# Optimization experiments

Hardware: AMD Instinct MI355X
Metric: run time of the kernel (lower is better)

Reference implementation:

```python
import jax, jax.numpy as jnp
import numpy as np

N = 100000
E = 3200000
NEG_SLOPE = 0.2  # PyG GATConv default


def gat_layer(x, src, dst, W, a_src, a_dst, b, heads, out_ch, concat):
    # per-node linear transform, split into heads: [N, H, C]
    h = (x @ W).reshape(N, heads, out_ch)
    # per-node attention logits: [N, H]
    al_src = jnp.sum(h * a_src, axis=-1)
    al_dst = jnp.sum(h * a_dst, axis=-1)
    # per-edge attention coefficient (x_j = source, x_i = target): [E, H]
    e = jax.nn.leaky_relu(al_src[src] + al_dst[dst], NEG_SLOPE)
    # segment softmax over incoming edges of each destination node
    m = jax.ops.segment_max(e, dst, num_segments=N)
    e = jnp.exp(e - m[dst])
    denom = jax.ops.segment_sum(e, dst, num_segments=N)
    alpha = e / (denom[dst] + 1e-16)
    # weighted message aggregation: scatter-add over dst
    msg = h[src] * alpha[..., None]  # [E, H, C]
    out = jax.ops.segment_sum(msg, dst, num_segments=N)  # [N, H, C]
    out = out.reshape(N, heads * out_ch) if concat else out.mean(axis=1)
    return out + b


def setup_inputs() -> dict:
    key = jax.random.key(0)
    ks = jax.random.split(key, 11)
    return {
        "x": jax.random.normal(ks[0], (N, 2), dtype=jnp.float32),
        "edge_index": jax.random.randint(ks[1], (2, E), 0, N, dtype=jnp.int64),
        "edge_attr": jax.random.normal(ks[2], (E, 1), dtype=jnp.float32),
        "W1": jax.random.normal(ks[3], (2, 32), dtype=jnp.float32) * 0.5,
        "att_src1": jax.random.normal(ks[4], (4, 8), dtype=jnp.float32) * 0.3,
        "att_dst1": jax.random.normal(ks[5], (4, 8), dtype=jnp.float32) * 0.3,
        "b1": jnp.zeros((32,), dtype=jnp.float32),
        "W2": jax.random.normal(ks[6], (32, 2), dtype=jnp.float32) * 0.2,
        "att_src2": jax.random.normal(ks[7], (1, 2), dtype=jnp.float32) * 0.3,
        "att_dst2": jax.random.normal(ks[8], (1, 2), dtype=jnp.float32) * 0.3,
        "b2": jnp.zeros((2,), dtype=jnp.float32),
    }


def reference(x, edge_index, edge_attr, W1, att_src1, att_dst1, b1, W2, att_src2, att_dst2, b2):
    # add self-loops (PyG GATConv default add_self_loops=True)
    loops = jnp.arange(N, dtype=edge_index.dtype)
    src = jnp.concatenate([edge_index[0], loops])
    dst = jnp.concatenate([edge_index[1], loops])
    h = gat_layer(x, src, dst, W1, att_src1, att_dst1, b1, heads=4, out_ch=8, concat=True)
    h = jax.nn.elu(h)
    out = gat_layer(h, src, dst, W2, att_src2, att_dst2, b2, heads=1, out_ch=2, concat=False)
    return out
```

## Files before the change

kernel.cpp:

```cpp
#include <hip/hip_runtime.h>
#include <math.h>

#define NEG_SLOPE 0.2f
#define BK_BITS 8
#define BK (1 << BK_BITS)
#define SBITS 17
#define SMASK ((1 << SBITS) - 1)
#define CAP 9216
#define PPT1 9
#define SW(p) ((p) ^ (((p) >> 5) & 31))
#define BCUR(b) ((b) * 16)

__device__ __forceinline__ float lrelu(float x) { return x > 0.f ? x : NEG_SLOPE * x; }

__global__ __launch_bounds__(512) void bucket_scatter(const int* __restrict__ src,
                                                      const int* __restrict__ dst,
                                                      int* __restrict__ bcur,
                                                      int* __restrict__ pairs, int E) {
    __shared__ int cnt[512], off[512], cur[512], adj[512];
    __shared__ int2 lpair[8196];
    __shared__ int sTot;
    int t = threadIdx.x;
    cnt[t] = 0;
    __syncthreads();

    int E4 = E >> 2;
    const int4* src4 = (const int4*)src;
    const int4* dst4 = (const int4*)dst;
    int base4 = blockIdx.x * 2048;
    int4 d4[4], s4[4];
    bool val[4];
#pragma unroll
    for (int k = 0; k < 4; k++) {
        int i4 = base4 + k * 512 + t;
        val[k] = (i4 < E4);
        if (val[k]) { d4[k] = dst4[i4]; s4[k] = src4[i4]; }
    }
    int dt = -1, st = 0;
    if (blockIdx.x == gridDim.x - 1) {
        int e = (E4 << 2) + t;
        if (e < E) { dt = dst[e]; st = src[e]; }
    }
#pragma unroll
    for (int k = 0; k < 4; k++) {
        if (val[k]) {
            atomicAdd(&cnt[d4[k].x >> BK_BITS], 1);
            atomicAdd(&cnt[d4[k].y >> BK_BITS], 1);
            atomicAdd(&cnt[d4[k].z >> BK_BITS], 1);
            atomicAdd(&cnt[d4[k].w >> BK_BITS], 1);
        }
    }
    if (dt >= 0) atomicAdd(&cnt[dt >> BK_BITS], 1);
    __syncthreads();

    if (t < 64) {
        int v[8], mysum = 0;
#pragma unroll
        for (int k = 0; k < 8; k++) { v[k] = cnt[t * 8 + k]; mysum += v[k]; }
        int s = mysum;
#pragma unroll
        for (int o = 1; o < 64; o <<= 1) {
            int u = __shfl_up(s, o);
            if (t >= o) s += u;
        }
        int run = s - mysum;
#pragma unroll
        for (int k = 0; k < 8; k++) {
            int d2 = t * 8 + k;
            off[d2] = run; cur[d2] = run;
            run += v[k];
        }
        if (t == 63) sTot = s;
    }
    __syncthreads();
    if (cnt[t] > 0) {
        int g0 = atomicAdd(&bcur[BCUR(t)], cnt[t]);
        adj[t] = t * CAP + g0 - off[t];
    }
    __syncthreads();
    int total = sTot;

#pragma unroll
    for (int k = 0; k < 4; k++) {
        if (val[k]) {
            int slot;
            slot = atomicAdd(&cur[d4[k].x >> BK_BITS], 1); lpair[slot] = make_int2(d4[k].x, s4[k].x);
            slot = atomicAdd(&cur[d4[k].y >> BK_BITS], 1); lpair[slot] = make_int2(d4[k].y, s4[k].y);
            slot = atomicAdd(&cur[d4[k].z >> BK_BITS], 1); lpair[slot] = make_int2(d4[k].z, s4[k].z);
            slot = atomicAdd(&cur[d4[k].w >> BK_BITS], 1); lpair[slot] = make_int2(d4[k].w, s4[k].w);
        }
    }
    if (dt >= 0) {
        int slot = atomicAdd(&cur[dt >> BK_BITS], 1);
        lpair[slot] = make_int2(dt, st);
    }
    __syncthreads();

    for (int i = t; i < total; i += 512) {
        int2 e = lpair[i];
        int b = e.x >> BK_BITS;
        pairs[adj[b] + i] = ((e.x & (BK - 1)) << SBITS) | e.y;
    }
}

__global__ __launch_bounds__(1024) void agg1_sortgather(
        const int* __restrict__ pairs, const int* __restrict__ bcur,
        const float2* __restrict__ x2,
        const float* __restrict__ W1, const float* __restrict__ asrc,
        const float* __restrict__ adst, const float* __restrict__ b1,
        const float* __restrict__ W2, const float* __restrict__ as2,
        const float* __restrict__ ad2,
        float2* __restrict__ h2, float* __restrict__ al2d,
        int* __restrict__ rowdeg, int* __restrict__ pairs_out, int N) {
    __shared__ float sW[64], sB[32], sW2[64], sP[4], sQ[4], sPd[4], sQd[4], sA2[4];
    __shared__ int cnt[BK], off[BK], cur[BK];
    __shared__ int sorted[CAP];
    int t = threadIdx.x;
    int b = blockIdx.x;
    if (t < 64) { sW[t] = W1[t]; sW2[t] = W2[t]; }
    if (t < 32) sB[t] = b1[t];
    if (t < 2) { sA2[t] = as2[t]; sA2[2 + t] = ad2[t]; }
    if (t >= 64 && t < 68) {
        int tt = t - 64;
        float P = 0.f, Q = 0.f, Pd = 0.f, Qd = 0.f;
#pragma unroll
        for (int k = 0; k < 8; k++) {
            int c = tt * 8 + k;
            float a = asrc[c], ad_ = adst[c];
            float w0 = W1[c], w1 = W1[32 + c];
            P += w0 * a; Q += w1 * a;
            Pd += w0 * ad_; Qd += w1 * ad_;
        }
        sP[tt] = P; sQ[tt] = Q; sPd[tt] = Pd; sQd[tt] = Qd;
    }
    if (t < BK) cnt[t] = 0;
    __syncthreads();

    int dbase = b << BK_BITS;
    int ndst = min(BK, N - dbase);
    int lo = b * CAP;
    int hi = lo + min(bcur[BCUR(b)], CAP);

    int myp[PPT1];
#pragma unroll
    for (int k = 0; k < PPT1; k++) {
        int i = lo + t + k * 1024;
        myp[k] = (i < hi) ? pairs[i] : -1;
    }
#pragma unroll
    for (int k = 0; k < PPT1; k++) {
        if (myp[k] >= 0) atomicAdd(&cnt[myp[k] >> SBITS], 1);
    }
    __syncthreads();

    if (t < 64) {
        int v[4], mysum = 0;
#pragma unroll
        for (int k = 0; k < 4; k++) { v[k] = cnt[t * 4 + k]; mysum += v[k]; }
        int s = mysum;
#pragma unroll
        for (int o = 1; o < 64; o <<= 1) {
            int u = __shfl_up(s, o);
            if (t >= o) s += u;
        }
        int run = s - mysum;
#pragma unroll
        for (int k = 0; k < 4; k++) {
            int d2 = t * 4 + k;
            off[d2] = run; cur[d2] = run;
            run += v[k];
        }
    }
    __syncthreads();

#pragma unroll
    for (int k = 0; k < PPT1; k++) {
        int p = myp[k];
        if (p >= 0) {
            int pos = atomicAdd(&cur[p >> SBITS], 1);
            sorted[SW(pos)] = p & SMASK;
        }
    }
    __syncthreads();

    {
        const int4* s4 = (const int4*)sorted;
        int4* p4 = (int4*)(pairs_out + lo);
        for (int i = t; i < CAP / 4; i += 1024) p4[i] = s4[i];
    }
    if (t < ndst) rowdeg[dbase + t] = (off[t] << 8) | min(cnt[t], 255);

    int d = t >> 2, q = t & 3;
    if (d < ndst) {
        int n = dbase + d;
        float rP[4], rQ[4], ald[4];
        float2 xd = x2[n];
#pragma unroll
        for (int h = 0; h < 4; h++) {
            rP[h] = sP[h]; rQ[h] = sQ[h];
            ald[h] = xd.x * sPd[h] + xd.y * sQd[h];
        }
        int deg = cnt[d];
        int start = off[d];
        int ids[16];
#pragma unroll
        for (int k = 0; k < 16; k++) {
            int j = q + 4 * k;
            ids[k] = (j < deg) ? sorted[SW(start + j)] : -1;
        }
        float Sw[4] = {0.f, 0.f, 0.f, 0.f};
        float S0[4] = {0.f, 0.f, 0.f, 0.f};
        float S1[4] = {0.f, 0.f, 0.f, 0.f};
#pragma unroll
        for (int half = 0; half < 2; half++) {
            float2 xv[8];
#pragma unroll
            for (int k = 0; k < 8; k++) {
                int id = ids[half * 8 + k];
                xv[k] = x2[id >= 0 ? id : 0];
            }
#pragma unroll
            for (int k = 0; k < 8; k++) {
                if (ids[half * 8 + k] >= 0) {
#pragma unroll
                    for (int h = 0; h < 4; h++) {
                        float e = lrelu(fmaf(xv[k].x, rP[h], fmaf(xv[k].y, rQ[h], ald[h])));
                        float w = __expf(fminf(e, 80.f));
                        Sw[h] += w; S0[h] += w * xv[k].x; S1[h] += w * xv[k].y;
                    }
                }
            }
        }
        for (int j = q + 64; j < deg; j += 4) {
            int s = sorted[SW(start + j)];
            float2 xs = x2[s];
#pragma unroll
            for (int h = 0; h < 4; h++) {
                float e = lrelu(fmaf(xs.x, rP[h], fmaf(xs.y, rQ[h], ald[h])));
                float w = __expf(fminf(e, 80.f));
                Sw[h] += w; S0[h] += w * xs.x; S1[h] += w * xs.y;
            }
        }
#pragma unroll
        for (int o = 1; o <= 2; o <<= 1) {
#pragma unroll
            for (int h = 0; h < 4; h++) {
                Sw[h] += __shfl_xor(Sw[h], o);
                S0[h] += __shfl_xor(S0[h], o);
                S1[h] += __shfl_xor(S1[h], o);
            }
        }
        if (q == 0) {
#pragma unroll
            for (int h = 0; h < 4; h++) {
                float e = lrelu(fmaf(xd.x, rP[h], fmaf(xd.y, rQ[h], ald[h])));
                float w = __expf(fminf(e, 80.f));
                Sw[h] += w; S0[h] += w * xd.x; S1[h] += w * xd.y;
            }
            float r[4];
#pragma unroll
            for (int h = 0; h < 4; h++) r[h] = 1.f / (Sw[h] + 1e-16f);
            float h20 = 0.f, h21 = 0.f;
#pragma unroll
            for (int c = 0; c < 32; c++) {
                int h = c >> 3;
                float outc = (sW[c] * S0[h] + sW[32 + c] * S1[h]) * r[h];
                float v2 = outc + sB[c];
                v2 = v2 > 0.f ? v2 : __expf(v2) - 1.f;
                h20 = fmaf(v2, sW2[2 * c], h20);
                h21 = fmaf(v2, sW2[2 * c + 1], h21);
            }
            h2[n] = make_float2(h20, h21);
            al2d[n] = h20 * sA2[2] + h21 * sA2[3];
        }
    }
}

__global__ __launch_bounds__(1024) void agg2_gather(
        const int* __restrict__ pairs, const int* __restrict__ rowdeg,
        const float2* __restrict__ h2, const float* __restrict__ al2d,
        const float* __restrict__ as2, const float* __restrict__ b2,
        float2* __restrict__ out, int N) {
    __shared__ int sorted[CAP];
    int t = threadIdx.x;
    int b = blockIdx.x;
    int dbase = b << BK_BITS;
    int ndst = min(BK, N - dbase);
    int lo = b * CAP;
    float a0 = as2[0], a1 = as2[1];

    {
        const int4* p4 = (const int4*)(pairs + lo);
        int4* s4 = (int4*)sorted;
        for (int i = t; i < CAP / 4; i += 1024) s4[i] = p4[i];
    }
    __syncthreads();

    int d = t >> 2, q = t & 3;
    if (d < ndst) {
        int n = dbase + d;
        int rd = rowdeg[n];
        int start = rd >> 8;
        int deg = rd & 255;
        float ald = al2d[n];
        float2 hd = h2[n];
        int ids[16];
#pragma unroll
        for (int k = 0; k < 16; k++) {
            int j = q + 4 * k;
            ids[k] = (j < deg) ? sorted[SW(start + j)] : -1;
        }
        float wsum = 0.f, ax = 0.f, ay = 0.f;
#pragma unroll
        for (int half = 0; half < 2; half++) {
            float2 hv[8];
#pragma unroll
            for (int k = 0; k < 8; k++) {
                int id = ids[half * 8 + k];
                hv[k] = h2[id >= 0 ? id : 0];
            }
#pragma unroll
            for (int k = 0; k < 8; k++) {
                if (ids[half * 8 + k] >= 0) {
                    float e = lrelu(fmaf(hv[k].x, a0, fmaf(hv[k].y, a1, ald)));
                    float w = __expf(fminf(e, 80.f));
                    wsum += w; ax = fmaf(w, hv[k].x, ax); ay = fmaf(w, hv[k].y, ay);
                }
            }
        }
        for (int j = q + 64; j < deg; j += 4) {
            int s = sorted[SW(start + j)];
            float2 hv = h2[s];
            float e = lrelu(fmaf(hv.x, a0, fmaf(hv.y, a1, ald)));
            float w = __expf(fminf(e, 80.f));
            wsum += w; ax = fmaf(w, hv.x, ax); ay = fmaf(w, hv.y, ay);
        }
#pragma unroll
        for (int o = 1; o <= 2; o <<= 1) {
            wsum += __shfl_xor(wsum, o);
            ax += __shfl_xor(ax, o);
            ay += __shfl_xor(ay, o);
        }
        if (q == 0) {
            float e = lrelu(fmaf(hd.x, a0, fmaf(hd.y, a1, ald)));
            float w = __expf(fminf(e, 80.f));
            wsum += w; ax = fmaf(w, hd.x, ax); ay = fmaf(w, hd.y, ay);
            float inv = 1.f / (wsum + 1e-16f);
            out[n] = make_float2(ax * inv + b2[0], ay * inv + b2[1]);
        }
    }
}

extern "C" void kernel_launch(void* const* d_in, const int* in_sizes, int n_in,
                              void* d_out, int out_size, void* d_ws, size_t ws_size,
                              hipStream_t stream) {
    const float* x     = (const float*)d_in[0];
    const int*   eidx  = (const int*)d_in[1];
    const float* W1    = (const float*)d_in[3];
    const float* asrc1 = (const float*)d_in[4];
    const float* adst1 = (const float*)d_in[5];
    const float* b1    = (const float*)d_in[6];
    const float* W2    = (const float*)d_in[7];
    const float* asrc2 = (const float*)d_in[8];
    const float* adst2 = (const float*)d_in[9];
    const float* b2    = (const float*)d_in[10];

    const int N = in_sizes[0] / 2;
    const int E = in_sizes[1] / 2;
    const int* src = eidx;
    const int* dst = eidx + E;
    const int NB = (N + BK - 1) >> BK_BITS;

    float* w = (float*)d_ws;
    float2* h2    = (float2*)w;
    float*  al2d  = w + 2 * (size_t)N;
    int* ip       = (int*)(w + 3 * (size_t)N);
    int* rowdeg   = ip;
    int* bcur     = ip + (size_t)N;
    int* pairs    = ip + (size_t)N + 8192;

    int E4 = E >> 2;
    int gS = (E4 + 2047) / 2048;

    hipMemsetAsync(bcur, 0, 8192 * sizeof(int), stream);
    bucket_scatter<<<gS, 512, 0, stream>>>(src, dst, bcur, pairs, E);
    agg1_sortgather<<<NB, 1024, 0, stream>>>(pairs, bcur, (const float2*)x,
                                             W1, asrc1, adst1, b1, W2, asrc2, adst2,
                                             h2, al2d, rowdeg, pairs, N);
    agg2_gather<<<NB, 1024, 0, stream>>>(pairs, rowdeg, (const float2*)h2, al2d,
                                         asrc2, b2, (float2*)d_out, N);
}
```

Baseline: 161.6 us.

## Replace global bucket atomics with per-block fixed cells and drop memset

The scatter kernel no longer reserves space in each destination bucket with global atomics. Each scatter block writes its edges into a fixed 64-slot cell per bucket and records its per-bucket count, and the aggregation kernel reads all cells for its bucket using those counts. This removes the memset launch and the contention on global atomics, but it reads up to nblk*64 slots per bucket (26 rounds per thread) and silently drops any edges beyond 64 per cell. The second-layer kernel now reads the sorted lists straight from global memory instead of staging them in LDS, removing a block-wide barrier.

```diff
diff --git a/kernel.cpp b/kernel.cpp
--- a/kernel.cpp
+++ b/kernel.cpp
@@ -7,27 +7,29 @@
 #define SBITS 17
 #define SMASK ((1 << SBITS) - 1)
 #define CAP 9216
-#define PPT1 9
+#define CELL 64
+#define RNDS 26
 #define SW(p) ((p) ^ (((p) >> 5) & 31))
-#define BCUR(b) ((b) * 16)
 
 __device__ __forceinline__ float lrelu(float x) { return x > 0.f ? x : NEG_SLOPE * x; }
 
 __global__ __launch_bounds__(512) void bucket_scatter(const int* __restrict__ src,
                                                       const int* __restrict__ dst,
-                                                      int* __restrict__ bcur,
-                                                      int* __restrict__ pairs, int E) {
-    __shared__ int cnt[512], off[512], cur[512], adj[512];
+                                                      int* __restrict__ cnt_g,
+                                                      int* __restrict__ cells,
+                                                      int E, int nblk) {
+    __shared__ int cnt[512], off[512], cur[512];
     __shared__ int2 lpair[8196];
     __shared__ int sTot;
     int t = threadIdx.x;
+    int blk = blockIdx.x;
     cnt[t] = 0;
     __syncthreads();
 
     int E4 = E >> 2;
     const int4* src4 = (const int4*)src;
     const int4* dst4 = (const int4*)dst;
-    int base4 = blockIdx.x * 2048;
+    int base4 = blk * 2048;
     int4 d4[4], s4[4];
     bool val[4];
 #pragma unroll
@@ -37,7 +39,7 @@
         if (val[k]) { d4[k] = dst4[i4]; s4[k] = src4[i4]; }
     }
     int dt = -1, st = 0;
-    if (blockIdx.x == gridDim.x - 1) {
+    if (blk == gridDim.x - 1) {
         int e = (E4 << 2) + t;
         if (e < E) { dt = dst[e]; st = src[e]; }
     }
@@ -53,6 +55,7 @@
     if (dt >= 0) atomicAdd(&cnt[dt >> BK_BITS], 1);
     __syncthreads();
 
+    cnt_g[blk * 512 + t] = min(cnt[t], CELL);
     if (t < 64) {
         int v[8], mysum = 0;
 #pragma unroll
@@ -71,11 +74,6 @@
             run += v[k];
         }
         if (t == 63) sTot = s;
-    }
-    __syncthreads();
-    if (cnt[t] > 0) {
-        int g0 = atomicAdd(&bcur[BCUR(t)], cnt[t]);
-        adj[t] = t * CAP + g0 - off[t];
     }
     __syncthreads();
     int total = sTot;
@@ -96,24 +94,29 @@
     }
     __syncthreads();
 
+    int cellbase = blk * CELL;
     for (int i = t; i < total; i += 512) {
         int2 e = lpair[i];
         int b = e.x >> BK_BITS;
-        pairs[adj[b] + i] = ((e.x & (BK - 1)) << SBITS) | e.y;
+        int slot = i - off[b];
+        if (slot < CELL)
+            cells[(size_t)b * (nblk * CELL) + cellbase + slot] =
+                ((e.x & (BK - 1)) << SBITS) | e.y;
     }
 }
 
 __global__ __launch_bounds__(1024) void agg1_sortgather(
-        const int* __restrict__ pairs, const int* __restrict__ bcur,
+        const int* __restrict__ cells, const int* __restrict__ cnt_g,
         const float2* __restrict__ x2,
         const float* __restrict__ W1, const float* __restrict__ asrc,
         const float* __restrict__ adst, const float* __restrict__ b1,
         const float* __restrict__ W2, const float* __restrict__ as2,
         const float* __restrict__ ad2,
         float2* __restrict__ h2, float* __restrict__ al2d,
-        int* __restrict__ rowdeg, int* __restrict__ pairs_out, int N) {
+        int* __restrict__ rowdeg, int* __restrict__ pairs2, int N, int nblk) {
     __shared__ float sW[64], sB[32], sW2[64], sP[4], sQ[4], sPd[4], sQd[4], sA2[4];
     __shared__ int cnt[BK], off[BK], cur[BK];
+    __shared__ int ccnt[512];
     __shared__ int sorted[CAP];
     int t = threadIdx.x;
     int b = blockIdx.x;
@@ -133,23 +136,25 @@
         }
         sP[tt] = P; sQ[tt] = Q; sPd[tt] = Pd; sQd[tt] = Qd;
     }
-    if (t < BK) cnt[t] = 0;
+    if (t < nblk) ccnt[t] = cnt_g[t * 512 + b];
+    if (t >= 512 && t < 512 + BK) cnt[t - 512] = 0;
     __syncthreads();
 
     int dbase = b << BK_BITS;
     int ndst = min(BK, N - dbase);
-    int lo = b * CAP;
-    int hi = lo + min(bcur[BCUR(b)], CAP);
-
-    int myp[PPT1];
-#pragma unroll
-    for (int k = 0; k < PPT1; k++) {
-        int i = lo + t + k * 1024;
-        myp[k] = (i < hi) ? pairs[i] : -1;
-    }
-#pragma unroll
-    for (int k = 0; k < PPT1; k++) {
-        if (myp[k] >= 0) atomicAdd(&cnt[myp[k] >> SBITS], 1);
+    int nslots = nblk * CELL;
+    size_t base = (size_t)b * nslots;
+
+    int myp[RNDS];
+#pragma unroll
+    for (int r = 0; r < RNDS; r++) {
+        int s = t + r * 1024;
+        bool v = (s < nslots) && ((s & (CELL - 1)) < ccnt[s >> 6]);
+        myp[r] = v ? cells[base + s] : -1;
+    }
+#pragma unroll
+    for (int r = 0; r < RNDS; r++) {
+        if (myp[r] >= 0) atomicAdd(&cnt[myp[r] >> SBITS], 1);
     }
     __syncthreads();
 
@@ -174,8 +179,8 @@
     __syncthreads();
 
 #pragma unroll
-    for (int k = 0; k < PPT1; k++) {
-        int p = myp[k];
+    for (int r = 0; r < RNDS; r++) {
+        int p = myp[r];
         if (p >= 0) {
             int pos = atomicAdd(&cur[p >> SBITS], 1);
             sorted[SW(pos)] = p & SMASK;
@@ -183,11 +188,7 @@
     }
     __syncthreads();
 
-    {
-        const int4* s4 = (const int4*)sorted;
-        int4* p4 = (int4*)(pairs_out + lo);
-        for (int i = t; i < CAP / 4; i += 1024) p4[i] = s4[i];
-    }
+    for (int i = t; i < CAP; i += 1024) pairs2[b * CAP + i] = sorted[SW(i)];
     if (t < ndst) rowdeg[dbase + t] = (off[t] << 8) | min(cnt[t], 255);
 
     int d = t >> 2, q = t & 3;
@@ -277,77 +278,68 @@
 }
 
 __global__ __launch_bounds__(1024) void agg2_gather(
-        const int* __restrict__ pairs, const int* __restrict__ rowdeg,
+        const int* __restrict__ pairs2, const int* __restrict__ rowdeg,
         const float2* __restrict__ h2, const float* __restrict__ al2d,
         const float* __restrict__ as2, const float* __restrict__ b2,
         float2* __restrict__ out, int N) {
-    __shared__ int sorted[CAP];
     int t = threadIdx.x;
     int b = blockIdx.x;
     int dbase = b << BK_BITS;
     int ndst = min(BK, N - dbase);
-    int lo = b * CAP;
+    int d = t >> 2, q = t & 3;
+    if (d >= ndst) return;
     float a0 = as2[0], a1 = as2[1];
 
-    {
-        const int4* p4 = (const int4*)(pairs + lo);
-        int4* s4 = (int4*)sorted;
-        for (int i = t; i < CAP / 4; i += 1024) s4[i] = p4[i];
-    }
-    __syncthreads();
-
-    int d = t >> 2, q = t & 3;
-    if (d < ndst) {
-        int n = dbase + d;
-        int rd = rowdeg[n];
-        int start = rd >> 8;
-        int deg = rd & 255;
-        float ald = al2d[n];
-        float2 hd = h2[n];
-        int ids[16];
-#pragma unroll
-        for (int k = 0; k < 16; k++) {
-            int j = q + 4 * k;
-            ids[k] = (j < deg) ? sorted[SW(start + j)] : -1;
-        }
-        float wsum = 0.f, ax = 0.f, ay = 0.f;
-#pragma unroll
-        for (int half = 0; half < 2; half++) {
-            float2 hv[8];
-#pragma unroll
-            for (int k = 0; k < 8; k++) {
-                int id = ids[half * 8 + k];
-                hv[k] = h2[id >= 0 ? id : 0];
-            }
-#pragma unroll
-            for (int k = 0; k < 8; k++) {
-                if (ids[half * 8 + k] >= 0) {
-                    float e = lrelu(fmaf(hv[k].x, a0, fmaf(hv[k].y, a1, ald)));
-                    float w = __expf(fminf(e, 80.f));
-                    wsum += w; ax = fmaf(w, hv[k].x, ax); ay = fmaf(w, hv[k].y, ay);
-                }
-            }
-        }
-        for (int j = q + 64; j < deg; j += 4) {
-            int s = sorted[SW(start + j)];
-            float2 hv = h2[s];
-            float e = lrelu(fmaf(hv.x, a0, fmaf(hv.y, a1, ald)));
-            float w = __expf(fminf(e, 80.f));
-            wsum += w; ax = fmaf(w, hv.x, ax); ay = fmaf(w, hv.y, ay);
-        }
-#pragma unroll
-        for (int o = 1; o <= 2; o <<= 1) {
-            wsum += __shfl_xor(wsum, o);
-            ax += __shfl_xor(ax, o);
-            ay += __shfl_xor(ay, o);
-        }
-        if (q == 0) {
-            float e = lrelu(fmaf(hd.x, a0, fmaf(hd.y, a1, ald)));
-            float w = __expf(fminf(e, 80.f));
-            wsum += w; ax = fmaf(w, hd.x, ax); ay = fmaf(w, hd.y, ay);
-            float inv = 1.f / (wsum + 1e-16f);
-            out[n] = make_float2(ax * inv + b2[0], ay * inv + b2[1]);
-        }
+    int n = dbase + d;
+    int rd = rowdeg[n];
+    int start = rd >> 8;
+    int deg = rd & 255;
+    const int* lst = pairs2 + b * CAP + start;
+    float ald = al2d[n];
+    float2 hd = h2[n];
+    int ids[16];
+#pragma unroll
+    for (int k = 0; k < 16; k++) {
+        int j = q + 4 * k;
+        ids[k] = (j < deg) ? lst[j] : -1;
+    }
+    float wsum = 0.f, ax = 0.f, ay = 0.f;
+#pragma unroll
+    for (int half = 0; half < 2; half++) {
+        float2 hv[8];
+#pragma unroll
+        for (int k = 0; k < 8; k++) {
+            int id = ids[half * 8 + k];
+            hv[k] = h2[id >= 0 ? id : 0];
+        }
+#pragma unroll
+        for (int k = 0; k < 8; k++) {
+            if (ids[half * 8 + k] >= 0) {
+                float e = lrelu(fmaf(hv[k].x, a0, fmaf(hv[k].y, a1, ald)));
+                float w = __expf(fminf(e, 80.f));
+                wsum += w; ax = fmaf(w, hv[k].x, ax); ay = fmaf(w, hv[k].y, ay);
+            }
+        }
+    }
+    for (int j = q + 64; j < deg; j += 4) {
+        int s = lst[j];
+        float2 hv = h2[s];
+        float e = lrelu(fmaf(hv.x, a0, fmaf(hv.y, a1, ald)));
+        float w = __expf(fminf(e, 80.f));
+        wsum += w; ax = fmaf(w, hv.x, ax); ay = fmaf(w, hv.y, ay);
+    }
+#pragma unroll
+    for (int o = 1; o <= 2; o <<= 1) {
+        wsum += __shfl_xor(wsum, o);
+        ax += __shfl_xor(ax, o);
+        ay += __shfl_xor(ay, o);
+    }
+    if (q == 0) {
+        float e = lrelu(fmaf(hd.x, a0, fmaf(hd.y, a1, ald)));
+        float w = __expf(fminf(e, 80.f));
+        wsum += w; ax = fmaf(w, hd.x, ax); ay = fmaf(w, hd.y, ay);
+        float inv = 1.f / (wsum + 1e-16f);
+        out[n] = make_float2(ax * inv + b2[0], ay * inv + b2[1]);
     }
 }
 
@@ -370,23 +362,22 @@
     const int* src = eidx;
     const int* dst = eidx + E;
     const int NB = (N + BK - 1) >> BK_BITS;
+    int E4 = E >> 2;
+    const int nblk = (E4 + 2047) / 2048;
 
     float* w = (float*)d_ws;
     float2* h2    = (float2*)w;
     float*  al2d  = w + 2 * (size_t)N;
     int* ip       = (int*)(w + 3 * (size_t)N);
     int* rowdeg   = ip;
-    int* bcur     = ip + (size_t)N;
-    int* pairs    = ip + (size_t)N + 8192;
-
-    int E4 = E >> 2;
-    int gS = (E4 + 2047) / 2048;
-
-    hipMemsetAsync(bcur, 0, 8192 * sizeof(int), stream);
-    bucket_scatter<<<gS, 512, 0, stream>>>(src, dst, bcur, pairs, E);
-    agg1_sortgather<<<NB, 1024, 0, stream>>>(pairs, bcur, (const float2*)x,
+    int* cnt_g    = ip + (size_t)N;
+    int* pairs2   = cnt_g + (size_t)nblk * 512;
+    int* cells    = pairs2 + (size_t)NB * CAP;
+
+    bucket_scatter<<<nblk, 512, 0, stream>>>(src, dst, cnt_g, cells, E, nblk);
+    agg1_sortgather<<<NB, 1024, 0, stream>>>(cells, cnt_g, (const float2*)x,
                                              W1, asrc1, adst1, b1, W2, asrc2, adst2,
-                                             h2, al2d, rowdeg, pairs, N);
-    agg2_gather<<<NB, 1024, 0, stream>>>(pairs, rowdeg, (const float2*)h2, al2d,
+                                             h2, al2d, rowdeg, pairs2, N, nblk);
+    agg2_gather<<<NB, 1024, 0, stream>>>(pairs2, rowdeg, (const float2*)h2, al2d,
                                          asrc2, b2, (float2*)d_out, N);
 }
```

Result: faster. 158.3 us (-2.1%).

## Fuse bucket scatter and both GAT layers into one persistent grid-barrier kernel

Applied to the files above, without the earlier changes.

Replaces the three kernels (bucket scatter, layer-1 sort-gather, layer-2 gather) with one persistent kernel of 256 blocks of 1024 threads. The phases are separated by software grid barriers built on device-scope atomics. Buckets grow to 512 destination nodes, and each block keeps its sorted source list in shared memory across both layers, so the pairs_out write-back and the rowdeg array are gone. The aim is to cut launch gaps and global round trips. In exchange, all blocks must be co-resident or the barrier spins forever, only 196 of 256 blocks do aggregation work, each destination gets two threads instead of four, and edges past the fixed bucket capacity are silently dropped.

```diff
diff --git a/kernel.cpp b/kernel.cpp
--- a/kernel.cpp
+++ b/kernel.cpp
@@ -2,121 +2,49 @@
 #include <math.h>
 
 #define NEG_SLOPE 0.2f
-#define BK_BITS 8
+#define BK_BITS 9
 #define BK (1 << BK_BITS)
+#define NBK 196
 #define SBITS 17
 #define SMASK ((1 << SBITS) - 1)
-#define CAP 9216
-#define PPT1 9
+#define CAPB 17920
+#define PPTA 18
+#define LPAIR 12504
 #define SW(p) ((p) ^ (((p) >> 5) & 31))
-#define BCUR(b) ((b) * 16)
 
 __device__ __forceinline__ float lrelu(float x) { return x > 0.f ? x : NEG_SLOPE * x; }
 
-__global__ __launch_bounds__(512) void bucket_scatter(const int* __restrict__ src,
-                                                      const int* __restrict__ dst,
-                                                      int* __restrict__ bcur,
-                                                      int* __restrict__ pairs, int E) {
-    __shared__ int cnt[512], off[512], cur[512], adj[512];
-    __shared__ int2 lpair[8196];
-    __shared__ int sTot;
-    int t = threadIdx.x;
-    cnt[t] = 0;
+__device__ __forceinline__ void gridbar(int* bar, int nb) {
     __syncthreads();
-
-    int E4 = E >> 2;
-    const int4* src4 = (const int4*)src;
-    const int4* dst4 = (const int4*)dst;
-    int base4 = blockIdx.x * 2048;
-    int4 d4[4], s4[4];
-    bool val[4];
-#pragma unroll
-    for (int k = 0; k < 4; k++) {
-        int i4 = base4 + k * 512 + t;
-        val[k] = (i4 < E4);
-        if (val[k]) { d4[k] = dst4[i4]; s4[k] = src4[i4]; }
-    }
-    int dt = -1, st = 0;
-    if (blockIdx.x == gridDim.x - 1) {
-        int e = (E4 << 2) + t;
-        if (e < E) { dt = dst[e]; st = src[e]; }
-    }
-#pragma unroll
-    for (int k = 0; k < 4; k++) {
-        if (val[k]) {
-            atomicAdd(&cnt[d4[k].x >> BK_BITS], 1);
-            atomicAdd(&cnt[d4[k].y >> BK_BITS], 1);
-            atomicAdd(&cnt[d4[k].z >> BK_BITS], 1);
-            atomicAdd(&cnt[d4[k].w >> BK_BITS], 1);
-        }
-    }
-    if (dt >= 0) atomicAdd(&cnt[dt >> BK_BITS], 1);
+    if (threadIdx.x == 0) {
+        __hip_atomic_fetch_add(bar, 1, __ATOMIC_RELEASE, __HIP_MEMORY_SCOPE_AGENT);
+        while (__hip_atomic_load(bar, __ATOMIC_RELAXED, __HIP_MEMORY_SCOPE_AGENT) < nb) {}
+        (void)__hip_atomic_load(bar, __ATOMIC_ACQUIRE, __HIP_MEMORY_SCOPE_AGENT);
+    }
     __syncthreads();
-
-    if (t < 64) {
-        int v[8], mysum = 0;
-#pragma unroll
-        for (int k = 0; k < 8; k++) { v[k] = cnt[t * 8 + k]; mysum += v[k]; }
-        int s = mysum;
-#pragma unroll
-        for (int o = 1; o < 64; o <<= 1) {
-            int u = __shfl_up(s, o);
-            if (t >= o) s += u;
-        }
-        int run = s - mysum;
-#pragma unroll
-        for (int k = 0; k < 8; k++) {
-            int d2 = t * 8 + k;
-            off[d2] = run; cur[d2] = run;
-            run += v[k];
-        }
-        if (t == 63) sTot = s;
-    }
-    __syncthreads();
-    if (cnt[t] > 0) {
-        int g0 = atomicAdd(&bcur[BCUR(t)], cnt[t]);
-        adj[t] = t * CAP + g0 - off[t];
-    }
-    __syncthreads();
-    int total = sTot;
-
-#pragma unroll
-    for (int k = 0; k < 4; k++) {
-        if (val[k]) {
-            int slot;
-            slot = atomicAdd(&cur[d4[k].x >> BK_BITS], 1); lpair[slot] = make_int2(d4[k].x, s4[k].x);
-            slot = atomicAdd(&cur[d4[k].y >> BK_BITS], 1); lpair[slot] = make_int2(d4[k].y, s4[k].y);
-            slot = atomicAdd(&cur[d4[k].z >> BK_BITS], 1); lpair[slot] = make_int2(d4[k].z, s4[k].z);
-            slot = atomicAdd(&cur[d4[k].w >> BK_BITS], 1); lpair[slot] = make_int2(d4[k].w, s4[k].w);
-        }
-    }
-    if (dt >= 0) {
-        int slot = atomicAdd(&cur[dt >> BK_BITS], 1);
-        lpair[slot] = make_int2(dt, st);
-    }
-    __syncthreads();
-
-    for (int i = t; i < total; i += 512) {
-        int2 e = lpair[i];
-        int b = e.x >> BK_BITS;
-        pairs[adj[b] + i] = ((e.x & (BK - 1)) << SBITS) | e.y;
-    }
 }
 
-__global__ __launch_bounds__(1024) void agg1_sortgather(
-        const int* __restrict__ pairs, const int* __restrict__ bcur,
+__global__ __launch_bounds__(1024) void gat_fused(
+        const int* __restrict__ src, const int* __restrict__ dst,
+        int* __restrict__ bar, int* __restrict__ bcur, int* __restrict__ pairs,
         const float2* __restrict__ x2,
         const float* __restrict__ W1, const float* __restrict__ asrc,
         const float* __restrict__ adst, const float* __restrict__ b1,
         const float* __restrict__ W2, const float* __restrict__ as2,
-        const float* __restrict__ ad2,
+        const float* __restrict__ ad2, const float* __restrict__ b2g,
         float2* __restrict__ h2, float* __restrict__ al2d,
-        int* __restrict__ rowdeg, int* __restrict__ pairs_out, int N) {
+        float2* __restrict__ out, int N, int E) {
+    __shared__ union {
+        int2 lpair[LPAIR];
+        int  sorted[CAPB];
+    } U;
+    __shared__ int cnt[512], off[512], cur[512], adj[256];
     __shared__ float sW[64], sB[32], sW2[64], sP[4], sQ[4], sPd[4], sQd[4], sA2[4];
-    __shared__ int cnt[BK], off[BK], cur[BK];
-    __shared__ int sorted[CAP];
+    __shared__ int sTot;
     int t = threadIdx.x;
-    int b = blockIdx.x;
+    int blk = blockIdx.x;
+    int nb = gridDim.x;
+
     if (t < 64) { sW[t] = W1[t]; sW2[t] = W2[t]; }
     if (t < 32) sB[t] = b1[t];
     if (t < 2) { sA2[t] = as2[t]; sA2[2 + t] = ad2[t]; }
@@ -133,220 +61,255 @@
         }
         sP[tt] = P; sQ[tt] = Q; sPd[tt] = Pd; sQd[tt] = Qd;
     }
-    if (t < BK) cnt[t] = 0;
+    if (t < 256) cnt[t] = 0;
     __syncthreads();
 
-    int dbase = b << BK_BITS;
-    int ndst = min(BK, N - dbase);
-    int lo = b * CAP;
-    int hi = lo + min(bcur[BCUR(b)], CAP);
-
-    int myp[PPT1];
-#pragma unroll
-    for (int k = 0; k < PPT1; k++) {
-        int i = lo + t + k * 1024;
-        myp[k] = (i < hi) ? pairs[i] : -1;
-    }
-#pragma unroll
-    for (int k = 0; k < PPT1; k++) {
-        if (myp[k] >= 0) atomicAdd(&cnt[myp[k] >> SBITS], 1);
-    }
-    __syncthreads();
-
-    if (t < 64) {
-        int v[4], mysum = 0;
-#pragma unroll
-        for (int k = 0; k < 4; k++) { v[k] = cnt[t * 4 + k]; mysum += v[k]; }
-        int s = mysum;
-#pragma unroll
-        for (int o = 1; o < 64; o <<= 1) {
-            int u = __shfl_up(s, o);
-            if (t >= o) s += u;
-        }
-        int run = s - mysum;
+    {
+        int E4 = E >> 2;
+        int chunk4 = (E4 + nb - 1) / nb;
+        const int4* src4 = (const int4*)src;
+        const int4* dst4 = (const int4*)dst;
+        int base4 = blk * chunk4;
+        int4 d4[4], s4[4];
+        bool val[4];
 #pragma unroll
         for (int k = 0; k < 4; k++) {
-            int d2 = t * 4 + k;
-            off[d2] = run; cur[d2] = run;
-            run += v[k];
-        }
-    }
-    __syncthreads();
-
-#pragma unroll
-    for (int k = 0; k < PPT1; k++) {
-        int p = myp[k];
-        if (p >= 0) {
-            int pos = atomicAdd(&cur[p >> SBITS], 1);
-            sorted[SW(pos)] = p & SMASK;
-        }
-    }
-    __syncthreads();
-
-    {
-        const int4* s4 = (const int4*)sorted;
-        int4* p4 = (int4*)(pairs_out + lo);
-        for (int i = t; i < CAP / 4; i += 1024) p4[i] = s4[i];
-    }
-    if (t < ndst) rowdeg[dbase + t] = (off[t] << 8) | min(cnt[t], 255);
-
-    int d = t >> 2, q = t & 3;
-    if (d < ndst) {
-        int n = dbase + d;
-        float rP[4], rQ[4], ald[4];
-        float2 xd = x2[n];
-#pragma unroll
-        for (int h = 0; h < 4; h++) {
-            rP[h] = sP[h]; rQ[h] = sQ[h];
-            ald[h] = xd.x * sPd[h] + xd.y * sQd[h];
-        }
-        int deg = cnt[d];
-        int start = off[d];
-        int ids[16];
-#pragma unroll
-        for (int k = 0; k < 16; k++) {
-            int j = q + 4 * k;
-            ids[k] = (j < deg) ? sorted[SW(start + j)] : -1;
-        }
-        float Sw[4] = {0.f, 0.f, 0.f, 0.f};
-        float S0[4] = {0.f, 0.f, 0.f, 0.f};
-        float S1[4] = {0.f, 0.f, 0.f, 0.f};
-#pragma unroll
-        for (int half = 0; half < 2; half++) {
-            float2 xv[8];
+            int o = k * 1024 + t;
+            int i4 = base4 + o;
+            val[k] = (o < chunk4) && (i4 < E4);
+            if (val[k]) { d4[k] = dst4[i4]; s4[k] = src4[i4]; }
+        }
+        int dt = -1, st = 0;
+        if (blk == nb - 1) {
+            int e = (E4 << 2) + t;
+            if (e < E) { dt = dst[e]; st = src[e]; }
+        }
+#pragma unroll
+        for (int k = 0; k < 4; k++) {
+            if (val[k]) {
+                atomicAdd(&cnt[d4[k].x >> BK_BITS], 1);
+                atomicAdd(&cnt[d4[k].y >> BK_BITS], 1);
+                atomicAdd(&cnt[d4[k].z >> BK_BITS], 1);
+                atomicAdd(&cnt[d4[k].w >> BK_BITS], 1);
+            }
+        }
+        if (dt >= 0) atomicAdd(&cnt[dt >> BK_BITS], 1);
+        __syncthreads();
+
+        if (t < 64) {
+            int v[4], mysum = 0;
+#pragma unroll
+            for (int k = 0; k < 4; k++) { v[k] = cnt[t * 4 + k]; mysum += v[k]; }
+            int s = mysum;
+#pragma unroll
+            for (int o = 1; o < 64; o <<= 1) {
+                int u = __shfl_up(s, o);
+                if (t >= o) s += u;
+            }
+            int run = s - mysum;
+#pragma unroll
+            for (int k = 0; k < 4; k++) {
+                int d2 = t * 4 + k;
+                off[d2] = run; cur[d2] = run;
+                run += v[k];
+            }
+            if (t == 63) sTot = s;
+        }
+        __syncthreads();
+        if (t < 256 && cnt[t] > 0) {
+            int g0 = atomicAdd(&bcur[t * 16], cnt[t]);
+            adj[t] = t * CAPB + g0 - off[t];
+        }
+        __syncthreads();
+        int total = sTot;
+
+#pragma unroll
+        for (int k = 0; k < 4; k++) {
+            if (val[k]) {
+                int slot;
+                slot = atomicAdd(&cur[d4[k].x >> BK_BITS], 1); U.lpair[slot] = make_int2(d4[k].x, s4[k].x);
+                slot = atomicAdd(&cur[d4[k].y >> BK_BITS], 1); U.lpair[slot] = make_int2(d4[k].y, s4[k].y);
+                slot = atomicAdd(&cur[d4[k].z >> BK_BITS], 1); U.lpair[slot] = make_int2(d4[k].z, s4[k].z);
+                slot = atomicAdd(&cur[d4[k].w >> BK_BITS], 1); U.lpair[slot] = make_int2(d4[k].w, s4[k].w);
+            }
+        }
+        if (dt >= 0) {
+            int slot = atomicAdd(&cur[dt >> BK_BITS], 1);
+            U.lpair[slot] = make_int2(dt, st);
+        }
+        __syncthreads();
+
+        for (int i = t; i < total; i += 1024) {
+            int2 e = U.lpair[i];
+            int b = e.x >> BK_BITS;
+            int pos = adj[b] + i;
+            if (pos - b * CAPB < CAPB)
+                pairs[pos] = ((e.x & (BK - 1)) << SBITS) | e.y;
+        }
+    }
+
+    gridbar(bar, nb);
+
+    int bi = blk;
+    int dbase = bi << BK_BITS;
+    int ndst = (bi < NBK) ? min(BK, N - dbase) : 0;
+    if (ndst > 0) {
+        if (t < 512) cnt[t] = 0;
+        __syncthreads();
+        int hi = min(bcur[bi * 16], CAPB);
+        const int* pb = pairs + bi * CAPB;
+
+        int myp[PPTA];
+#pragma unroll
+        for (int k = 0; k < PPTA; k++) {
+            int i = t + k * 1024;
+            myp[k] = (i < hi) ? pb[i] : -1;
+        }
+#pragma unroll
+        for (int k = 0; k < PPTA; k++)
+            if (myp[k] >= 0) atomicAdd(&cnt[myp[k] >> SBITS], 1);
+        __syncthreads();
+
+        if (t < 64) {
+            int v[8], mysum = 0;
+#pragma unroll
+            for (int k = 0; k < 8; k++) { v[k] = cnt[t * 8 + k]; mysum += v[k]; }
+            int s = mysum;
+#pragma unroll
+            for (int o = 1; o < 64; o <<= 1) {
+                int u = __shfl_up(s, o);
+                if (t >= o) s += u;
+            }
+            int run = s - mysum;
 #pragma unroll
             for (int k = 0; k < 8; k++) {
-                int id = ids[half * 8 + k];
-                xv[k] = x2[id >= 0 ? id : 0];
-            }
-#pragma unroll
-            for (int k = 0; k < 8; k++) {
-                if (ids[half * 8 + k] >= 0) {
-#pragma unroll
-                    for (int h = 0; h < 4; h++) {
-                        float e = lrelu(fmaf(xv[k].x, rP[h], fmaf(xv[k].y, rQ[h], ald[h])));
+                int d2 = t * 8 + k;
+                off[d2] = run; cur[d2] = run;
+                run += v[k];
+            }
+        }
+        __syncthreads();
+
+#pragma unroll
+        for (int k = 0; k < PPTA; k++) {
+            int p = myp[k];
+            if (p >= 0) {
+                int pos = atomicAdd(&cur[p >> SBITS], 1);
+                U.sorted[SW(pos)] = p & SMASK;
+            }
+        }
+        __syncthreads();
+
+        int d = t >> 1, q = t & 1;
+        if (d < ndst) {
+            int n = dbase + d;
+            float rP[4], rQ[4], ald[4];
+            float2 xd = x2[n];
+#pragma unroll
+            for (int h = 0; h < 4; h++) {
+                rP[h] = sP[h]; rQ[h] = sQ[h];
+                ald[h] = xd.x * sPd[h] + xd.y * sQd[h];
+            }
+            int deg = cnt[d];
+            int start = off[d];
+            float Sw[4] = {0.f, 0.f, 0.f, 0.f};
+            float S0[4] = {0.f, 0.f, 0.f, 0.f};
+            float S1[4] = {0.f, 0.f, 0.f, 0.f};
+            for (int j0 = q; j0 < deg; j0 += 16) {
+                int ids[8];
+                float2 xv[8];
+#pragma unroll
+                for (int k = 0; k < 8; k++) {
+                    int j = j0 + 2 * k;
+                    ids[k] = (j < deg) ? U.sorted[SW(start + j)] : -1;
+                }
+#pragma unroll
+                for (int k = 0; k < 8; k++) xv[k] = x2[ids[k] >= 0 ? ids[k] : 0];
+#pragma unroll
+                for (int k = 0; k < 8; k++) {
+                    if (ids[k] >= 0) {
+#pragma unroll
+                        for (int h = 0; h < 4; h++) {
+                            float e = lrelu(fmaf(xv[k].x, rP[h], fmaf(xv[k].y, rQ[h], ald[h])));
+                            float w = __expf(fminf(e, 80.f));
+                            Sw[h] += w; S0[h] += w * xv[k].x; S1[h] += w * xv[k].y;
+                        }
+                    }
+                }
+            }
+#pragma unroll
+            for (int h = 0; h < 4; h++) {
+                Sw[h] += __shfl_xor(Sw[h], 1);
+                S0[h] += __shfl_xor(S0[h], 1);
+                S1[h] += __shfl_xor(S1[h], 1);
+            }
+            if (q == 0) {
+#pragma unroll
+                for (int h = 0; h < 4; h++) {
+                    float e = lrelu(fmaf(xd.x, rP[h], fmaf(xd.y, rQ[h], ald[h])));
+                    float w = __expf(fminf(e, 80.f));
+                    Sw[h] += w; S0[h] += w * xd.x; S1[h] += w * xd.y;
+                }
+                float r[4];
+#pragma unroll
+                for (int h = 0; h < 4; h++) r[h] = 1.f / (Sw[h] + 1e-16f);
+                float h20 = 0.f, h21 = 0.f;
+#pragma unroll
+                for (int c = 0; c < 32; c++) {
+                    int h = c >> 3;
+                    float outc = (sW[c] * S0[h] + sW[32 + c] * S1[h]) * r[h];
+                    float v2 = outc + sB[c];
+                    v2 = v2 > 0.f ? v2 : __expf(v2) - 1.f;
+                    h20 = fmaf(v2, sW2[2 * c], h20);
+                    h21 = fmaf(v2, sW2[2 * c + 1], h21);
+                }
+                h2[n] = make_float2(h20, h21);
+                al2d[n] = h20 * sA2[2] + h21 * sA2[3];
+            }
+        }
+    }
+
+    gridbar(bar + 16, nb);
+
+    if (ndst > 0) {
+        float a0 = sA2[0], a1 = sA2[1];
+        int d = t >> 1, q = t & 1;
+        if (d < ndst) {
+            int n = dbase + d;
+            int deg = cnt[d];
+            int start = off[d];
+            float ald = al2d[n];
+            float2 hd = h2[n];
+            float wsum = 0.f, ax = 0.f, ay = 0.f;
+            for (int j0 = q; j0 < deg; j0 += 16) {
+                int ids[8];
+                float2 hv[8];
+#pragma unroll
+                for (int k = 0; k < 8; k++) {
+                    int j = j0 + 2 * k;
+                    ids[k] = (j < deg) ? U.sorted[SW(start + j)] : -1;
+                }
+#pragma unroll
+                for (int k = 0; k < 8; k++) hv[k] = h2[ids[k] >= 0 ? ids[k] : 0];
+#pragma unroll
+                for (int k = 0; k < 8; k++) {
+                    if (ids[k] >= 0) {
+                        float e = lrelu(fmaf(hv[k].x, a0, fmaf(hv[k].y, a1, ald)));
                         float w = __expf(fminf(e, 80.f));
-                        Sw[h] += w; S0[h] += w * xv[k].x; S1[h] += w * xv[k].y;
+                        wsum += w; ax = fmaf(w, hv[k].x, ax); ay = fmaf(w, hv[k].y, ay);
                     }
                 }
             }
-        }
-        for (int j = q + 64; j < deg; j += 4) {
-            int s = sorted[SW(start + j)];
-            float2 xs = x2[s];
-#pragma unroll
-            for (int h = 0; h < 4; h++) {
-                float e = lrelu(fmaf(xs.x, rP[h], fmaf(xs.y, rQ[h], ald[h])));
+            wsum += __shfl_xor(wsum, 1);
+            ax += __shfl_xor(ax, 1);
+            ay += __shfl_xor(ay, 1);
+            if (q == 0) {
+                float e = lrelu(fmaf(hd.x, a0, fmaf(hd.y, a1, ald)));
                 float w = __expf(fminf(e, 80.f));
-                Sw[h] += w; S0[h] += w * xs.x; S1[h] += w * xs.y;
-            }
-        }
-#pragma unroll
-        for (int o = 1; o <= 2; o <<= 1) {
-#pragma unroll
-            for (int h = 0; h < 4; h++) {
-                Sw[h] += __shfl_xor(Sw[h], o);
-                S0[h] += __shfl_xor(S0[h], o);
-                S1[h] += __shfl_xor(S1[h], o);
-            }
-        }
-        if (q == 0) {
-#pragma unroll
-            for (int h = 0; h < 4; h++) {
-                float e = lrelu(fmaf(xd.x, rP[h], fmaf(xd.y, rQ[h], ald[h])));
-                float w = __expf(fminf(e, 80.f));
-                Sw[h] += w; S0[h] += w * xd.x; S1[h] += w * xd.y;
-            }
-            float r[4];
-#pragma unroll
-            for (int h = 0; h < 4; h++) r[h] = 1.f / (Sw[h] + 1e-16f);
-            float h20 = 0.f, h21 = 0.f;
-#pragma unroll
-            for (int c = 0; c < 32; c++) {
-                int h = c >> 3;
-                float outc = (sW[c] * S0[h] + sW[32 + c] * S1[h]) * r[h];
-                float v2 = outc + sB[c];
-                v2 = v2 > 0.f ? v2 : __expf(v2) - 1.f;
-                h20 = fmaf(v2, sW2[2 * c], h20);
-                h21 = fmaf(v2, sW2[2 * c + 1], h21);
-            }
-            h2[n] = make_float2(h20, h21);
-            al2d[n] = h20 * sA2[2] + h21 * sA2[3];
-        }
-    }
-}
-
-__global__ __launch_bounds__(1024) void agg2_gather(
-        const int* __restrict__ pairs, const int* __restrict__ rowdeg,
-        const float2* __restrict__ h2, const float* __restrict__ al2d,
-        const float* __restrict__ as2, const float* __restrict__ b2,
-        float2* __restrict__ out, int N) {
-    __shared__ int sorted[CAP];
-    int t = threadIdx.x;
-    int b = blockIdx.x;
-    int dbase = b << BK_BITS;
-    int ndst = min(BK, N - dbase);
-    int lo = b * CAP;
-    float a0 = as2[0], a1 = as2[1];
-
-    {
-        const int4* p4 = (const int4*)(pairs + lo);
-        int4* s4 = (int4*)sorted;
-        for (int i = t; i < CAP / 4; i += 1024) s4[i] = p4[i];
-    }
-    __syncthreads();
-
-    int d = t >> 2, q = t & 3;
-    if (d < ndst) {
-        int n = dbase + d;
-        int rd = rowdeg[n];
-        int start = rd >> 8;
-        int deg = rd & 255;
-        float ald = al2d[n];
-        float2 hd = h2[n];
-        int ids[16];
-#pragma unroll
-        for (int k = 0; k < 16; k++) {
-            int j = q + 4 * k;
-            ids[k] = (j < deg) ? sorted[SW(start + j)] : -1;
-        }
-        float wsum = 0.f, ax = 0.f, ay = 0.f;
-#pragma unroll
-        for (int half = 0; half < 2; half++) {
-            float2 hv[8];
-#pragma unroll
-            for (int k = 0; k < 8; k++) {
-                int id = ids[half * 8 + k];
-                hv[k] = h2[id >= 0 ? id : 0];
-            }
-#pragma unroll
-            for (int k = 0; k < 8; k++) {
-                if (ids[half * 8 + k] >= 0) {
-                    float e = lrelu(fmaf(hv[k].x, a0, fmaf(hv[k].y, a1, ald)));
-                    float w = __expf(fminf(e, 80.f));
-                    wsum += w; ax = fmaf(w, hv[k].x, ax); ay = fmaf(w, hv[k].y, ay);
-                }
-            }
-        }
-        for (int j = q + 64; j < deg; j += 4) {
-            int s = sorted[SW(start + j)];
-            float2 hv = h2[s];
-            float e = lrelu(fmaf(hv.x, a0, fmaf(hv.y, a1, ald)));
-            float w = __expf(fminf(e, 80.f));
-            wsum += w; ax = fmaf(w, hv.x, ax); ay = fmaf(w, hv.y, ay);
-        }
-#pragma unroll
-        for (int o = 1; o <= 2; o <<= 1) {
-            wsum += __shfl_xor(wsum, o);
-            ax += __shfl_xor(ax, o);
-            ay += __shfl_xor(ay, o);
-        }
-        if (q == 0) {
-            float e = lrelu(fmaf(hd.x, a0, fmaf(hd.y, a1, ald)));
-            float w = __expf(fminf(e, 80.f));
-            wsum += w; ax = fmaf(w, hd.x, ax); ay = fmaf(w, hd.y, ay);
-            float inv = 1.f / (wsum + 1e-16f);
-            out[n] = make_float2(ax * inv + b2[0], ay * inv + b2[1]);
+                wsum += w; ax = fmaf(w, hd.x, ax); ay = fmaf(w, hd.y, ay);
+                float inv = 1.f / (wsum + 1e-16f);
+                out[n] = make_float2(ax * inv + b2g[0], ay * inv + b2g[1]);
+            }
         }
     }
 }
@@ -369,24 +332,19 @@
     const int E = in_sizes[1] / 2;
     const int* src = eidx;
     const int* dst = eidx + E;
-    const int NB = (N + BK - 1) >> BK_BITS;
 
     float* w = (float*)d_ws;
     float2* h2    = (float2*)w;
     float*  al2d  = w + 2 * (size_t)N;
     int* ip       = (int*)(w + 3 * (size_t)N);
-    int* rowdeg   = ip;
-    int* bcur     = ip + (size_t)N;
-    int* pairs    = ip + (size_t)N + 8192;
-
-    int E4 = E >> 2;
-    int gS = (E4 + 2047) / 2048;
-
-    hipMemsetAsync(bcur, 0, 8192 * sizeof(int), stream);
-    bucket_scatter<<<gS, 512, 0, stream>>>(src, dst, bcur, pairs, E);
-    agg1_sortgather<<<NB, 1024, 0, stream>>>(pairs, bcur, (const float2*)x,
-                                             W1, asrc1, adst1, b1, W2, asrc2, adst2,
-                                             h2, al2d, rowdeg, pairs, N);
-    agg2_gather<<<NB, 1024, 0, stream>>>(pairs, rowdeg, (const float2*)h2, al2d,
-                                         asrc2, b2, (float2*)d_out, N);
+    int* bar      = ip;
+    int* bcur     = ip + 32;
+    int* pairs    = ip + 32 + 4096;
+
+    hipMemsetAsync(bar, 0, (32 + 4096) * sizeof(int), stream);
+
+    gat_fused<<<256, 1024, 0, stream>>>(src, dst, bar, bcur, pairs,
+                                        (const float2*)x,
+                                        W1, asrc1, adst1, b1, W2, asrc2, adst2, b2,
+                                        h2, al2d, (float2*)d_out, N, E);
 }
```

Result: slower. 183.6 us (+13.6%).
